# Performance work log

Measured on AMD Instinct MI355X. Metric: run time of the kernel, lower is better.

The kernel has to match this reference:

```python
import jax, jax.numpy as jnp
import numpy as np

K = 10          # hardcoded in module (self.K = 10)
H = 26          # neighbors per query point in this run
PAD_H = 28      # layer_ind2neighbor[layer_ind=0]
KP_EXTENT = 1.2 # linear-influence extent


def setup_inputs() -> dict:
    key = jax.random.key(0)
    ks = jax.random.split(key, 6)
    N, Ns, Cin, Cout = 65536, 65536, 64, 128
    q_pts = jax.random.normal(ks[0], (N, 3), jnp.float32)
    s_pts = jax.random.normal(ks[1], (Ns, 3), jnp.float32)
    neighb_inds = jax.random.randint(ks[2], (N, H), 0, Ns)
    x = jax.random.normal(ks[3], (Ns, Cin), jnp.float32)
    # kernel_points_generator: Linear(PAD_H*3 -> K*3)
    gen_W = jax.random.normal(ks[4], (K * 3, PAD_H * 3), jnp.float32) * (1.0 / np.sqrt(PAD_H * 3))
    gen_b = jnp.zeros((K * 3,), jnp.float32)
    # KPConv weights: [K, in, out] (kaiming_uniform in torch; scaled normal here)
    weights = jax.random.normal(ks[5], (K, Cin, Cout), jnp.float32) * (1.0 / np.sqrt(Cin))
    return {"q_pts": q_pts, "s_pts": s_pts, "x": x,
            "gen_W": gen_W, "gen_b": gen_b, "weights": weights,
            "neighb_inds": neighb_inds}


def _kpconv(q_pts, s_pts, x, gen_W, gen_b, weights, neighb_inds):
    N = q_pts.shape[0]
    # shadow support point far away (index Ns)
    s_pad = jnp.concatenate([s_pts, jnp.full((1, 3), 1e6, s_pts.dtype)], axis=0)
    neighbors = s_pad[neighb_inds] - q_pts[:, None, :]                          # [N,H,3]
    # generative kernel points: pad neighbor list with -1 up to PAD_H, run linear
    padded = jnp.concatenate(
        [neighbors, jnp.full((N, PAD_H - H, 3), -1.0, neighbors.dtype)], axis=1)
    kp = (padded.reshape(N, -1) @ gen_W.T + gen_b).reshape(N, 1, K, 3)          # [N,1,K,3]
    diff = neighbors[:, :, None, :] - kp                                        # [N,H,K,3]
    sq_d = jnp.sum(diff * diff, axis=3)                                         # [N,H,K]
    # KP_influence == 'linear'
    all_w = jnp.maximum(1.0 - jnp.sqrt(sq_d) / KP_EXTENT, 0.0)
    all_w = jnp.swapaxes(all_w, 1, 2)                                           # [N,K,H]
    # shadow feature row (zeros) at index Ns
    x_pad = jnp.concatenate([x, jnp.zeros((1, x.shape[1]), x.dtype)], axis=0)
    neighb_x = x_pad[neighb_inds]                                               # [N,H,Cin]
    weighted = jnp.einsum('nkh,nhi->nki', all_w, neighb_x)                      # [N,K,Cin]
    return jnp.einsum('nki,kio->no', weighted, weights)                         # [N,Cout]


def reference(q_pts, s_pts, x, gen_W, gen_b, weights, neighb_inds):
    return _kpconv(q_pts, s_pts, x, gen_W, gen_b, weights, neighb_inds)
```

## Files before the change

kernel.cpp:

```cpp
#include <hip/hip_runtime.h>
#include <stdint.h>

#define N_Q   65536
#define N_S   65536
#define NB_H  26
#define PAD_H 28
#define KP    10
#define CIN   64
#define COUT  128
#define MT    8
#define BM    32
#define NPASS (BM / MT)
#define LDA   648

typedef unsigned short u16x8  __attribute__((ext_vector_type(8)));
typedef float          f32x4  __attribute__((ext_vector_type(4)));
typedef _Float16       f16x8  __attribute__((ext_vector_type(8)));
typedef _Float16       f16x2  __attribute__((ext_vector_type(2)));

#define CVT_BLOCKS 2049
#define PACK_BLOCKS 40

static __device__ __forceinline__ unsigned short f2h(float f) {
  return __builtin_bit_cast(unsigned short, (_Float16)f);
}

static __device__ __forceinline__ unsigned int pkrtz_u32(float a, float b) {
  return __builtin_bit_cast(unsigned int, __builtin_amdgcn_cvt_pkrtz(a, b));
}

static __device__ __forceinline__ float fdot2u(unsigned int a, unsigned int b, float c) {
#if __has_builtin(__builtin_amdgcn_fdot2)
  return __builtin_amdgcn_fdot2(__builtin_bit_cast(f16x2, a),
                                __builtin_bit_cast(f16x2, b), c, false);
#else
  f16x2 ha = __builtin_bit_cast(f16x2, a), hb = __builtin_bit_cast(f16x2, b);
  return c + (float)ha[0] * (float)hb[0] + (float)ha[1] * (float)hb[1];
#endif
}

__global__ void prep_kernel(const float* __restrict__ x,
                            const float* __restrict__ w,
                            unsigned short* __restrict__ xh,
                            unsigned short* __restrict__ bp) {
  if (blockIdx.x < CVT_BLOCKS) {
    long t = (long)blockIdx.x * blockDim.x + threadIdx.x;
    long off = t * 8;
    if (off >= (long)(N_S + 1) * CIN) return;
    u16x8 o;
    if (off < (long)N_S * CIN) {
      f32x4 a = *(const f32x4*)(x + off);
      f32x4 b = *(const f32x4*)(x + off + 4);
      o[0] = f2h(a[0]); o[1] = f2h(a[1]); o[2] = f2h(a[2]); o[3] = f2h(a[3]);
      o[4] = f2h(b[0]); o[5] = f2h(b[1]); o[6] = f2h(b[2]); o[7] = f2h(b[3]);
    } else {
      o = (u16x8)0;
    }
    *(u16x8*)(xh + off) = o;
  } else {
    int t = (blockIdx.x - CVT_BLOCKS) * blockDim.x + threadIdx.x;
    if (t >= 8 * 20 * 64) return;
    int lane = t & 63;
    int frag = t >> 6;
    int ks = frag % 20;
    int ct = frag / 20;
    int row0 = ks * 32 + (lane >> 4) * 8;
    int col  = ct * 16 + (lane & 15);
    u16x8 o;
    #pragma unroll
    for (int j = 0; j < 8; ++j) o[j] = f2h(w[(row0 + j) * COUT + col]);
    *(u16x8*)(bp + (long)t * 8) = o;
  }
}

__global__ void __launch_bounds__(256, 3)
kpconv_fused(const float* __restrict__ q_pts, const float* __restrict__ s_pts,
             const float* __restrict__ gen_W, const float* __restrict__ gen_b,
             const int* __restrict__ inds, const unsigned short* __restrict__ xh,
             const unsigned short* __restrict__ bp, float* __restrict__ out) {

  __shared__ int            sh_ind[MT][NB_H];
  __shared__ float          sh_nbr[MT][80];
  __shared__ float          sh_kp[MT][KP * 3];
  __shared__ unsigned int   sh_aw[MT][13][12];
  __shared__ unsigned short sA[BM][LDA];

  const int  tid  = threadIdx.x;
  const long row0 = (long)blockIdx.x * BM;

  #pragma unroll 1
  for (int pass = 0; pass < NPASS; ++pass) {
    const int pbase = (int)row0 + pass * MT;

    if (tid < MT * NB_H) {
      int m = tid / NB_H, h = tid % NB_H;
      int n = pbase + m;
      int ind = inds[n * NB_H + h];
      sh_ind[m][h] = ind;
      float sx, sy, sz;
      if ((unsigned)ind < (unsigned)N_S) {
        sx = s_pts[ind * 3 + 0]; sy = s_pts[ind * 3 + 1]; sz = s_pts[ind * 3 + 2];
      } else {
        sx = 1e6f; sy = 1e6f; sz = 1e6f;
      }
      sh_nbr[m][h * 3 + 0] = sx - q_pts[n * 3 + 0];
      sh_nbr[m][h * 3 + 1] = sy - q_pts[n * 3 + 1];
      sh_nbr[m][h * 3 + 2] = sz - q_pts[n * 3 + 2];
    }
    if (tid < MT * 2) sh_nbr[tid >> 1][78 + (tid & 1)] = -1.0f;
    __syncthreads();

    if (tid < MT * KP * 3) {
      int m = tid / 30, r = tid % 30;
      const float* Wr = gen_W + r * (PAD_H * 3);
      const f32x4* W4 = (const f32x4*)Wr;
      const f32x4* N4 = (const f32x4*)&sh_nbr[m][0];
      f32x4 accv = {0.f, 0.f, 0.f, 0.f};
      #pragma unroll
      for (int j = 0; j < 20; ++j) accv += W4[j] * N4[j];
      sh_kp[m][r] = gen_b[r] - (Wr[80] + Wr[81] + Wr[82] + Wr[83])
                  + accv[0] + accv[1] + accv[2] + accv[3];
    }
    __syncthreads();

    for (int p = tid; p < MT * 13 * KP; p += 256) {
      int k = p % KP;
      int t = p / KP;
      int m = t & (MT - 1);
      int hp = t >> 3;
      float kx = sh_kp[m][k * 3 + 0], ky = sh_kp[m][k * 3 + 1], kz = sh_kp[m][k * 3 + 2];
      int h0 = hp * 2;
      float dx0 = sh_nbr[m][h0 * 3 + 0] - kx;
      float dy0 = sh_nbr[m][h0 * 3 + 1] - ky;
      float dz0 = sh_nbr[m][h0 * 3 + 2] - kz;
      float w0 = fmaxf(1.0f - sqrtf(dx0 * dx0 + dy0 * dy0 + dz0 * dz0) * (1.0f / 1.2f), 0.0f);
      float dx1 = sh_nbr[m][h0 * 3 + 3] - kx;
      float dy1 = sh_nbr[m][h0 * 3 + 4] - ky;
      float dz1 = sh_nbr[m][h0 * 3 + 5] - kz;
      float w1 = fmaxf(1.0f - sqrtf(dx1 * dx1 + dy1 * dy1 + dz1 * dz1) * (1.0f / 1.2f), 0.0f);
      sh_aw[m][hp][k] = pkrtz_u32(w0, w1);
    }
    __syncthreads();

    {
      const int m  = tid >> 5;
      const int i0 = (tid & 31) * 2;
      float acc0[KP], acc1[KP];
      #pragma unroll
      for (int k = 0; k < KP; ++k) { acc0[k] = 0.f; acc1[k] = 0.f; }

      unsigned int xr[4];
      #pragma unroll
      for (int h = 0; h < 4; ++h)
        xr[h] = *(const unsigned int*)(xh + (long)sh_ind[m][h] * CIN + i0);

      #pragma unroll
      for (int p = 0; p < 13; ++p) {
        unsigned int r0 = xr[(2 * p) & 3];
        unsigned int r1 = xr[(2 * p + 1) & 3];
        if (2 * p + 4 < NB_H)
          xr[(2 * p) & 3] = *(const unsigned int*)(xh + (long)sh_ind[m][2 * p + 4] * CIN + i0);
        if (2 * p + 5 < NB_H)
          xr[(2 * p + 1) & 3] = *(const unsigned int*)(xh + (long)sh_ind[m][2 * p + 5] * CIN + i0);
        unsigned int pair0 = __builtin_amdgcn_perm(r1, r0, 0x05040100u);
        unsigned int pair1 = __builtin_amdgcn_perm(r1, r0, 0x07060302u);
        const unsigned int* wrow = &sh_aw[m][p][0];
        #pragma unroll
        for (int k = 0; k < KP; ++k) {
          unsigned int w2 = wrow[k];
          acc0[k] = fdot2u(w2, pair0, acc0[k]);
          acc1[k] = fdot2u(w2, pair1, acc1[k]);
        }
      }
      unsigned short* rowp = &sA[pass * MT + m][0];
      #pragma unroll
      for (int k = 0; k < KP; ++k)
        *(unsigned int*)(rowp + k * CIN + i0) = pkrtz_u32(acc0[k], acc1[k]);
    }
    __syncthreads();
  }

  {
    const int wave = tid >> 6;
    const int lane = tid & 63;
    const int ct0  = wave * 2, ct1 = ct0 + 1;
    const int arow = lane & 15;
    const int aq   = lane >> 4;

    f32x4 acc[2][2];
    #pragma unroll
    for (int rt = 0; rt < 2; ++rt)
      #pragma unroll
      for (int c = 0; c < 2; ++c) acc[rt][c] = (f32x4){0.f, 0.f, 0.f, 0.f};

    u16x8 pb0[4], pb1[4];
    #pragma unroll
    for (int d = 0; d < 4; ++d) {
      pb0[d] = *(const u16x8*)(bp + (long)((ct0 * 20 + d) * 64 + lane) * 8);
      pb1[d] = *(const u16x8*)(bp + (long)((ct1 * 20 + d) * 64 + lane) * 8);
    }

    #pragma unroll
    for (int ks = 0; ks < 20; ++ks) {
      f16x8 b0 = __builtin_bit_cast(f16x8, pb0[ks & 3]);
      f16x8 b1 = __builtin_bit_cast(f16x8, pb1[ks & 3]);
      if (ks + 4 < 20) {
        pb0[ks & 3] = *(const u16x8*)(bp + (long)((ct0 * 20 + ks + 4) * 64 + lane) * 8);
        pb1[ks & 3] = *(const u16x8*)(bp + (long)((ct1 * 20 + ks + 4) * 64 + lane) * 8);
      }
      #pragma unroll
      for (int rt = 0; rt < 2; ++rt) {
        u16x8 au = *(const u16x8*)&sA[rt * 16 + arow][ks * 32 + aq * 8];
        f16x8 a = __builtin_bit_cast(f16x8, au);
        acc[rt][0] = __builtin_amdgcn_mfma_f32_16x16x32_f16(a, b0, acc[rt][0], 0, 0, 0);
        acc[rt][1] = __builtin_amdgcn_mfma_f32_16x16x32_f16(a, b1, acc[rt][1], 0, 0, 0);
      }
    }

    const int col   = lane & 15;
    const int rbase = aq * 4;
    #pragma unroll
    for (int rt = 0; rt < 2; ++rt)
      #pragma unroll
      for (int r = 0; r < 4; ++r) {
        long row = row0 + rt * 16 + rbase + r;
        __builtin_nontemporal_store(acc[rt][0][r], &out[row * COUT + ct0 * 16 + col]);
        __builtin_nontemporal_store(acc[rt][1][r], &out[row * COUT + ct1 * 16 + col]);
      }
  }
}

extern "C" void kernel_launch(void* const* d_in, const int* in_sizes, int n_in,
                              void* d_out, int out_size, void* d_ws, size_t ws_size,
                              hipStream_t stream) {
  const float* q_pts = (const float*)d_in[0];
  const float* s_pts = (const float*)d_in[1];
  const float* x     = (const float*)d_in[2];
  const float* gen_W = (const float*)d_in[3];
  const float* gen_b = (const float*)d_in[4];
  const float* wts   = (const float*)d_in[5];
  const int*   inds  = (const int*)d_in[6];
  float* out = (float*)d_out;

  unsigned short* xh = (unsigned short*)d_ws;
  unsigned short* bp = xh + (size_t)(N_S + 1) * CIN;

  prep_kernel<<<CVT_BLOCKS + PACK_BLOCKS, 256, 0, stream>>>(x, wts, xh, bp);
  kpconv_fused<<<N_Q / BM, 256, 0, stream>>>(q_pts, s_pts, gen_W, gen_b,
                                             inds, xh, bp, out);
}
```

Baseline: 182.0 us.

## Halve rows per block, swizzle LDS A-tile, deepen gather prefetch for occupancy

Cuts rows per block from 32 to 16, which halves the LDS A-tile and lets launch bounds target 5 blocks per CU instead of 3. The A-tile is stored in a fragment-major layout, so each lane's MFMA operand read becomes one contiguous 16-byte LDS load with no padding. The gather prefetch window for neighbor feature rows goes from 4 to 8 registers to hide more memory latency. The cost is that each block now loads the full B weight fragments for only 16 rows, doubling B traffic per output row, and there is more register pressure under a tighter launch bound.

New measurement: 174.1 us. 1.05x faster.

```diff
diff --git a/kernel.cpp b/kernel.cpp
--- a/kernel.cpp
+++ b/kernel.cpp
@@ -9,9 +9,8 @@
 #define CIN   64
 #define COUT  128
 #define MT    8
-#define BM    32
+#define BM    16
 #define NPASS (BM / MT)
-#define LDA   648
 
 typedef unsigned short u16x8  __attribute__((ext_vector_type(8)));
 typedef float          f32x4  __attribute__((ext_vector_type(4)));
@@ -73,7 +72,7 @@
   }
 }
 
-__global__ void __launch_bounds__(256, 3)
+__global__ void __launch_bounds__(256, 5)
 kpconv_fused(const float* __restrict__ q_pts, const float* __restrict__ s_pts,
              const float* __restrict__ gen_W, const float* __restrict__ gen_b,
              const int* __restrict__ inds, const unsigned short* __restrict__ xh,
@@ -83,7 +82,7 @@
   __shared__ float          sh_nbr[MT][80];
   __shared__ float          sh_kp[MT][KP * 3];
   __shared__ unsigned int   sh_aw[MT][13][12];
-  __shared__ unsigned short sA[BM][LDA];
+  __shared__ unsigned short sA[20 * 512];
 
   const int  tid  = threadIdx.x;
   const long row0 = (long)blockIdx.x * BM;
@@ -149,19 +148,19 @@
       #pragma unroll
       for (int k = 0; k < KP; ++k) { acc0[k] = 0.f; acc1[k] = 0.f; }
 
-      unsigned int xr[4];
-      #pragma unroll
-      for (int h = 0; h < 4; ++h)
+      unsigned int xr[8];
+      #pragma unroll
+      for (int h = 0; h < 8; ++h)
         xr[h] = *(const unsigned int*)(xh + (long)sh_ind[m][h] * CIN + i0);
 
       #pragma unroll
       for (int p = 0; p < 13; ++p) {
-        unsigned int r0 = xr[(2 * p) & 3];
-        unsigned int r1 = xr[(2 * p + 1) & 3];
-        if (2 * p + 4 < NB_H)
-          xr[(2 * p) & 3] = *(const unsigned int*)(xh + (long)sh_ind[m][2 * p + 4] * CIN + i0);
-        if (2 * p + 5 < NB_H)
-          xr[(2 * p + 1) & 3] = *(const unsigned int*)(xh + (long)sh_ind[m][2 * p + 5] * CIN + i0);
+        unsigned int r0 = xr[(2 * p) & 7];
+        unsigned int r1 = xr[(2 * p + 1) & 7];
+        if (2 * p + 8 < NB_H)
+          xr[(2 * p) & 7] = *(const unsigned int*)(xh + (long)sh_ind[m][2 * p + 8] * CIN + i0);
+        if (2 * p + 9 < NB_H)
+          xr[(2 * p + 1) & 7] = *(const unsigned int*)(xh + (long)sh_ind[m][2 * p + 9] * CIN + i0);
         unsigned int pair0 = __builtin_amdgcn_perm(r1, r0, 0x05040100u);
         unsigned int pair1 = __builtin_amdgcn_perm(r1, r0, 0x07060302u);
         const unsigned int* wrow = &sh_aw[m][p][0];
@@ -172,10 +171,14 @@
           acc1[k] = fdot2u(w2, pair1, acc1[k]);
         }
       }
-      unsigned short* rowp = &sA[pass * MT + m][0];
+      const int row  = pass * MT + m;
+      const int qhi  = i0 >> 5;
+      const int e    = i0 & 31;
+      const int slot = row * 4 + (e >> 3);
+      const int hoff = slot * 8 + (e & 7);
       #pragma unroll
       for (int k = 0; k < KP; ++k)
-        *(unsigned int*)(rowp + k * CIN + i0) = pkrtz_u32(acc0[k], acc1[k]);
+        *(unsigned int*)(sA + (k * 2 + qhi) * 512 + hoff) = pkrtz_u32(acc0[k], acc1[k]);
     }
     __syncthreads();
   }
@@ -184,14 +187,11 @@
     const int wave = tid >> 6;
     const int lane = tid & 63;
     const int ct0  = wave * 2, ct1 = ct0 + 1;
-    const int arow = lane & 15;
-    const int aq   = lane >> 4;
-
-    f32x4 acc[2][2];
-    #pragma unroll
-    for (int rt = 0; rt < 2; ++rt)
-      #pragma unroll
-      for (int c = 0; c < 2; ++c) acc[rt][c] = (f32x4){0.f, 0.f, 0.f, 0.f};
+    const int aoff = ((lane & 15) * 4 + (lane >> 4)) * 8;
+
+    f32x4 acc[2];
+    acc[0] = (f32x4){0.f, 0.f, 0.f, 0.f};
+    acc[1] = (f32x4){0.f, 0.f, 0.f, 0.f};
 
     u16x8 pb0[4], pb1[4];
     #pragma unroll
@@ -208,25 +208,20 @@
         pb0[ks & 3] = *(const u16x8*)(bp + (long)((ct0 * 20 + ks + 4) * 64 + lane) * 8);
         pb1[ks & 3] = *(const u16x8*)(bp + (long)((ct1 * 20 + ks + 4) * 64 + lane) * 8);
       }
-      #pragma unroll
-      for (int rt = 0; rt < 2; ++rt) {
-        u16x8 au = *(const u16x8*)&sA[rt * 16 + arow][ks * 32 + aq * 8];
-        f16x8 a = __builtin_bit_cast(f16x8, au);
-        acc[rt][0] = __builtin_amdgcn_mfma_f32_16x16x32_f16(a, b0, acc[rt][0], 0, 0, 0);
-        acc[rt][1] = __builtin_amdgcn_mfma_f32_16x16x32_f16(a, b1, acc[rt][1], 0, 0, 0);
-      }
+      u16x8 au = *(const u16x8*)&sA[ks * 512 + aoff];
+      f16x8 a = __builtin_bit_cast(f16x8, au);
+      acc[0] = __builtin_amdgcn_mfma_f32_16x16x32_f16(a, b0, acc[0], 0, 0, 0);
+      acc[1] = __builtin_amdgcn_mfma_f32_16x16x32_f16(a, b1, acc[1], 0, 0, 0);
     }
 
     const int col   = lane & 15;
-    const int rbase = aq * 4;
-    #pragma unroll
-    for (int rt = 0; rt < 2; ++rt)
-      #pragma unroll
-      for (int r = 0; r < 4; ++r) {
-        long row = row0 + rt * 16 + rbase + r;
-        __builtin_nontemporal_store(acc[rt][0][r], &out[row * COUT + ct0 * 16 + col]);
-        __builtin_nontemporal_store(acc[rt][1][r], &out[row * COUT + ct1 * 16 + col]);
-      }
+    const int rbase = (lane >> 4) * 4;
+    #pragma unroll
+    for (int r = 0; r < 4; ++r) {
+      long row = row0 + rbase + r;
+      __builtin_nontemporal_store(acc[0][r], &out[row * COUT + ct0 * 16 + col]);
+      __builtin_nontemporal_store(acc[1][r], &out[row * COUT + ct1 * 16 + col]);
+    }
   }
 }
 
```
